# Kernel optimization log

Hardware: AMD Instinct MI355X
Metric: run time of the kernel (lower is better)

The kernel has to match this reference:

```python
import jax, jax.numpy as jnp
import numpy as np

P, L, D, H, K = 128, 800, 200, 100, 2  # passages, seq_len, input dim, hidden, spans per passage
VOCAB = 30522


def setup_inputs() -> dict:
    key = jax.random.key(0)
    ks = jax.random.split(key, 8)
    S_p = jax.random.normal(ks[0], (P, L, D), dtype=jnp.float32)
    # sorted along last axis so start <= end
    spans = jnp.sort(jax.random.randint(ks[1], (P, K, 2), 0, L), axis=-1)
    passages = jax.random.randint(ks[2], (P, L), 0, VOCAB)
    s = 0.05
    Wb = jax.random.normal(ks[3], (H, D), jnp.float32) * s
    We = jax.random.normal(ks[4], (H, D), jnp.float32) * s
    Wc = jax.random.normal(ks[5], (H, H), jnp.float32) * s
    Wo = jax.random.normal(ks[6], (H, H), jnp.float32) * s
    Wv = jax.random.normal(ks[7], (1, H), jnp.float32) * s
    return {"S_p": S_p, "spans": spans, "passages": passages,
            "Wb": Wb, "We": We, "Wc": Wc, "Wo": Wo, "Wv": Wv}


def reference(S_p, spans, passages, Wb, We, Wc, Wo, Wv):
    M = P * K
    p_idx = jnp.repeat(jnp.arange(P), K)            # [M] passage index per candidate
    starts = spans[:, :, 0].reshape(M)
    ends = spans[:, :, 1].reshape(M)
    t = jnp.arange(L)

    # S_Cs: candidate kept at its original position, zero elsewhere (== F.pad of the slice)
    span_mask = (t[None, :] >= starts[:, None]) & (t[None, :] <= ends[:, None])  # [M, L]
    S_Cs = S_p[p_idx] * span_mask[..., None].astype(S_p.dtype)                   # [M, L, D]

    # encoded candidates: token ids shifted to position 0, right-padded with 0
    gidx = jnp.clip(starts[:, None] + t[None, :], 0, L - 1)                      # [M, L]
    len_mask = t[None, :] <= (ends - starts)[:, None]
    encoded_candidates = jnp.where(len_mask, passages[p_idx[:, None], gidx], 0)  # [M, L]

    # condensed representation from start/end token states
    sb = S_p[p_idx, starts]                          # [M, D]
    se = S_p[p_idx, ends]                            # [M, D]
    r_Cs = jnp.tanh(sb @ Wb.T + se @ We.T)           # [M, H]

    # pairwise scores V_full[i, j] = Wv tanh(Wc r_i + Wo r_j)
    c = r_Cs @ Wc.T                                  # [M, H]
    o = r_Cs @ Wo.T                                  # [M, H]
    V_full = jnp.tanh(c[:, None, :] + o[None, :, :]) @ Wv[0]   # [M, M]

    # leave-one-out gather: V[i] = V_full[i, j != i]
    cols = jnp.arange(M - 1)
    rows = jnp.arange(M)
    idx = cols[None, :] + (cols[None, :] >= rows[:, None]).astype(cols.dtype)    # [M, M-1]
    V = V_full[rows[:, None], idx]                   # [M, M-1]

    # alpha[i] = exp(V[i]) / sum_{j != i} exp(V[j])  (per-column, non-standard normalization)
    E = jnp.exp(V)                                   # [M, M-1]
    denom = E.sum(axis=0, keepdims=True) - E
    alpha = E / denom                                # [M, M-1]

    # tilda_r[i] = sum over rows of (alpha excl row i) @ (r_Cs excl row i)
    s_rows = alpha.sum(axis=0, keepdims=True) - alpha   # [M, M-1]
    R_excl = r_Cs[idx]                                  # [M, M-1, H]
    tilda_r_Cs = jnp.einsum('mb,mbh->mh', s_rows, R_excl)  # [M, H]

    return S_Cs, r_Cs, encoded_candidates, V, tilda_r_Cs
```

## Files before the change

kernel.cpp:

```cpp
#include <hip/hip_runtime.h>
#include <math.h>

#define LP 800
#define DP 200
#define HP 100
#define MP 256
#define MM1 255

typedef float fx4 __attribute__((ext_vector_type(4)));

#define OFF_SCS  0u
#define OFF_R    40960000u
#define OFF_ENC  40985600u
#define OFF_V    41190400u
#define OFF_TIL  41255680u

#define WS_C     0u
#define WS_O     25600u
#define WS_S     51200u

__device__ __forceinline__ float tanh_fast(float x) {
    float e = __expf(2.0f * x);
    return 1.0f - 2.0f / (e + 1.0f);
}

__global__ __launch_bounds__(256) void scs_kernel(const fx4* __restrict__ Sp4,
                                                  const int* __restrict__ spans,
                                                  fx4* __restrict__ out4) {
    int m = blockIdx.y;
    int off = blockIdx.x * blockDim.x + threadIdx.x;
    if (off >= 40000) return;
    int p = m >> 1, k = m & 1;
    int start = spans[p * 4 + k * 2];
    int end   = spans[p * 4 + k * 2 + 1];
    int t = off / 50;
    fx4 v = (fx4)(0.f);
    if (t >= start && t <= end) v = Sp4[p * 40000 + off];
    __builtin_nontemporal_store(v, &out4[m * 40000 + off]);
}

__global__ __launch_bounds__(256) void encrco_kernel(const float* __restrict__ Sp,
                                                     const int* __restrict__ spans,
                                                     const int* __restrict__ passages,
                                                     const float* __restrict__ Wb,
                                                     const float* __restrict__ We,
                                                     const float* __restrict__ Wc,
                                                     const float* __restrict__ Wo,
                                                     float* __restrict__ enc,
                                                     float* __restrict__ r_out,
                                                     float* __restrict__ c_ws,
                                                     float* __restrict__ o_ws) {
    __shared__ float4 sb4[50], se4[50], rs4[25];
    int m = blockIdx.x;
    int p = m >> 1, k = m & 1;
    int start = spans[p * 4 + k * 2];
    int end   = spans[p * 4 + k * 2 + 1];
    int tid = threadIdx.x;

    int len = end - start;
    for (int t = tid; t < LP; t += 256) {
        int g = start + t; if (g > LP - 1) g = LP - 1;
        enc[m * LP + t] = (t <= len) ? (float)passages[p * LP + g] : 0.f;
    }

    const float4* sbp = (const float4*)(Sp + (size_t)(p * LP + start) * DP);
    const float4* sep = (const float4*)(Sp + (size_t)(p * LP + end) * DP);
    if (tid < 50)       sb4[tid]      = sbp[tid];
    else if (tid < 100) se4[tid - 50] = sep[tid - 50];
    __syncthreads();

    int h = tid;
    if (h < HP) {
        const float4* wb = (const float4*)(Wb + h * DP);
        const float4* we = (const float4*)(We + h * DP);
        float acc = 0.f;
        #pragma unroll
        for (int d = 0; d < 50; ++d) {
            float4 a = sb4[d], b = wb[d];
            acc += a.x * b.x + a.y * b.y + a.z * b.z + a.w * b.w;
            float4 a2 = se4[d], b2 = we[d];
            acc += a2.x * b2.x + a2.y * b2.y + a2.z * b2.z + a2.w * b2.w;
        }
        float r = tanh_fast(acc);
        ((float*)rs4)[h] = r;
        r_out[m * HP + h] = r;
    }
    __syncthreads();
    if (h < HP) {
        const float4* wc = (const float4*)(Wc + h * HP);
        const float4* wo = (const float4*)(Wo + h * HP);
        float accc = 0.f, acco = 0.f;
        #pragma unroll
        for (int q = 0; q < 25; ++q) {
            float4 r = rs4[q], cc = wc[q], oo = wo[q];
            accc += r.x * cc.x + r.y * cc.y + r.z * cc.z + r.w * cc.w;
            acco += r.x * oo.x + r.y * oo.y + r.z * oo.z + r.w * oo.w;
        }
        c_ws[m * HP + h] = accc;
        o_ws[m * HP + h] = acco;
    }
}

__global__ __launch_bounds__(256) void vcol_kernel(const float* __restrict__ c_ws,
                                                   const float* __restrict__ o_ws,
                                                   const float* __restrict__ Wv,
                                                   float* __restrict__ V_out,
                                                   float* __restrict__ s_ws) {
    __shared__ float4 olo4[25], ohi4[25], wv4[25];
    __shared__ float part[4];
    int jp = blockIdx.x;
    int i = threadIdx.x;
    if (i < 25) {
        olo4[i] = ((const float4*)(o_ws + jp * HP))[i];
        ohi4[i] = ((const float4*)(o_ws + (jp + 1) * HP))[i];
        wv4[i]  = ((const float4*)Wv)[i];
    }
    __syncthreads();

    const float4* c4p = (const float4*)(c_ws + i * HP);
    bool hi = (jp >= i);
    float acc = 0.f;
    #pragma unroll
    for (int q = 0; q < 25; ++q) {
        float4 c4 = c4p[q];
        float4 o4 = hi ? ohi4[q] : olo4[q];
        float4 w4 = wv4[q];
        acc += tanh_fast(c4.x + o4.x) * w4.x;
        acc += tanh_fast(c4.y + o4.y) * w4.y;
        acc += tanh_fast(c4.z + o4.z) * w4.z;
        acc += tanh_fast(c4.w + o4.w) * w4.w;
    }
    V_out[i * MM1 + jp] = acc;
    float e = __expf(acc);

    float v = e;
    v += __shfl_down(v, 32); v += __shfl_down(v, 16); v += __shfl_down(v, 8);
    v += __shfl_down(v, 4);  v += __shfl_down(v, 2);  v += __shfl_down(v, 1);
    if ((i & 63) == 0) part[i >> 6] = v;
    __syncthreads();
    float colE = part[0] + part[1] + part[2] + part[3];

    float a = e / (colE - e);

    __syncthreads();
    float v2 = a;
    v2 += __shfl_down(v2, 32); v2 += __shfl_down(v2, 16); v2 += __shfl_down(v2, 8);
    v2 += __shfl_down(v2, 4);  v2 += __shfl_down(v2, 2);  v2 += __shfl_down(v2, 1);
    if ((i & 63) == 0) part[i >> 6] = v2;
    __syncthreads();
    float colA = part[0] + part[1] + part[2] + part[3];

    s_ws[i * MM1 + jp] = colA - a;
}

__global__ __launch_bounds__(128) void tilda_kernel(const float* __restrict__ s_ws,
                                                    const float* __restrict__ r_out,
                                                    float* __restrict__ til_out) {
    __shared__ float s[MM1 + 1];
    int i = blockIdx.x;
    for (int jp = threadIdx.x; jp < MM1; jp += 128)
        s[jp] = s_ws[i * MM1 + jp];
    __syncthreads();
    int h = threadIdx.x;
    if (h < HP) {
        float acc = 0.f;
        #pragma unroll 4
        for (int jp = 0; jp < i; ++jp)
            acc += s[jp] * r_out[jp * HP + h];
        #pragma unroll 4
        for (int jp = i; jp < MM1; ++jp)
            acc += s[jp] * r_out[(jp + 1) * HP + h];
        til_out[i * HP + h] = acc;
    }
}

extern "C" void kernel_launch(void* const* d_in, const int* in_sizes, int n_in,
                              void* d_out, int out_size, void* d_ws, size_t ws_size,
                              hipStream_t stream) {
    const float* S_p      = (const float*)d_in[0];
    const int*   spans    = (const int*)d_in[1];
    const int*   passages = (const int*)d_in[2];
    const float* Wb       = (const float*)d_in[3];
    const float* We       = (const float*)d_in[4];
    const float* Wc       = (const float*)d_in[5];
    const float* Wo       = (const float*)d_in[6];
    const float* Wv       = (const float*)d_in[7];

    float* out = (float*)d_out;
    float* ws  = (float*)d_ws;

    float* out_scs = out + OFF_SCS;
    float* out_r   = out + OFF_R;
    float* out_enc = out + OFF_ENC;
    float* out_v   = out + OFF_V;
    float* out_til = out + OFF_TIL;

    float* ws_c = ws + WS_C;
    float* ws_o = ws + WS_O;
    float* ws_s = ws + WS_S;

    encrco_kernel<<<MP, 256, 0, stream>>>(S_p, spans, passages, Wb, We, Wc, Wo,
                                          out_enc, out_r, ws_c, ws_o);
    vcol_kernel<<<MM1, 256, 0, stream>>>(ws_c, ws_o, Wv, out_v, ws_s);
    tilda_kernel<<<MP, 128, 0, stream>>>(ws_s, out_r, out_til);

    dim3 gridA((40000 + 255) / 256, MP);
    scs_kernel<<<gridA, 256, 0, stream>>>((const fx4*)S_p, spans, (fx4*)out_scs);
}
```

Baseline: 276.9 us.

## Split S_Cs copy across the three dependent kernels to overlap small stages

Removes the standalone S_Cs masking kernel and spreads its 40000 blocks (one per 256 float4 writes) across the three dependent small kernels as extra blocks. The aim is to hide the latency-bound, low-occupancy encoder, pairwise-score and tilda stages behind the large bandwidth-bound copy. It also cuts one launch. The cost is per-element division to recover the candidate and offset from a flat index, and tilda blocks now run with 256 threads instead of 128.

```diff
diff --git a/kernel.cpp b/kernel.cpp
--- a/kernel.cpp
+++ b/kernel.cpp
@@ -19,37 +19,50 @@
 #define WS_O     25600u
 #define WS_S     51200u
 
+#define SCS_B1 13334
+#define SCS_B2 13333
+#define SCS_B3 13333
+#define NB1 0
+#define NB2 13334
+#define NB3 26667
+
 __device__ __forceinline__ float tanh_fast(float x) {
     float e = __expf(2.0f * x);
     return 1.0f - 2.0f / (e + 1.0f);
 }
 
-__global__ __launch_bounds__(256) void scs_kernel(const fx4* __restrict__ Sp4,
-                                                  const int* __restrict__ spans,
-                                                  fx4* __restrict__ out4) {
-    int m = blockIdx.y;
-    int off = blockIdx.x * blockDim.x + threadIdx.x;
-    if (off >= 40000) return;
-    int p = m >> 1, k = m & 1;
+__device__ __forceinline__ void scs_slice(const fx4* __restrict__ Sp4,
+                                          const int* __restrict__ spans,
+                                          fx4* __restrict__ out4,
+                                          unsigned ubase) {
+    unsigned u = ubase * 256u + threadIdx.x;
+    unsigned m = u / 40000u;
+    unsigned off = u - m * 40000u;
+    unsigned p = m >> 1, k = m & 1;
     int start = spans[p * 4 + k * 2];
     int end   = spans[p * 4 + k * 2 + 1];
-    int t = off / 50;
+    int t = (int)(off / 50u);
     fx4 v = (fx4)(0.f);
-    if (t >= start && t <= end) v = Sp4[p * 40000 + off];
-    __builtin_nontemporal_store(v, &out4[m * 40000 + off]);
-}
-
-__global__ __launch_bounds__(256) void encrco_kernel(const float* __restrict__ Sp,
-                                                     const int* __restrict__ spans,
-                                                     const int* __restrict__ passages,
-                                                     const float* __restrict__ Wb,
-                                                     const float* __restrict__ We,
-                                                     const float* __restrict__ Wc,
-                                                     const float* __restrict__ Wo,
-                                                     float* __restrict__ enc,
-                                                     float* __restrict__ r_out,
-                                                     float* __restrict__ c_ws,
-                                                     float* __restrict__ o_ws) {
+    if (t >= start && t <= end) v = Sp4[p * 40000u + off];
+    __builtin_nontemporal_store(v, &out4[m * 40000u + off]);
+}
+
+__global__ __launch_bounds__(256) void node1_kernel(const float* __restrict__ Sp,
+                                                    const int* __restrict__ spans,
+                                                    const int* __restrict__ passages,
+                                                    const float* __restrict__ Wb,
+                                                    const float* __restrict__ We,
+                                                    const float* __restrict__ Wc,
+                                                    const float* __restrict__ Wo,
+                                                    float* __restrict__ enc,
+                                                    float* __restrict__ r_out,
+                                                    float* __restrict__ c_ws,
+                                                    float* __restrict__ o_ws,
+                                                    fx4* __restrict__ out4) {
+    if (blockIdx.x >= MP) {
+        scs_slice((const fx4*)Sp, spans, out4, NB1 + blockIdx.x - MP);
+        return;
+    }
     __shared__ float4 sb4[50], se4[50], rs4[25];
     int m = blockIdx.x;
     int p = m >> 1, k = m & 1;
@@ -101,11 +114,18 @@
     }
 }
 
-__global__ __launch_bounds__(256) void vcol_kernel(const float* __restrict__ c_ws,
-                                                   const float* __restrict__ o_ws,
-                                                   const float* __restrict__ Wv,
-                                                   float* __restrict__ V_out,
-                                                   float* __restrict__ s_ws) {
+__global__ __launch_bounds__(256) void node2_kernel(const float* __restrict__ Sp,
+                                                    const int* __restrict__ spans,
+                                                    const float* __restrict__ c_ws,
+                                                    const float* __restrict__ o_ws,
+                                                    const float* __restrict__ Wv,
+                                                    float* __restrict__ V_out,
+                                                    float* __restrict__ s_ws,
+                                                    fx4* __restrict__ out4) {
+    if (blockIdx.x >= MM1) {
+        scs_slice((const fx4*)Sp, spans, out4, NB2 + blockIdx.x - MM1);
+        return;
+    }
     __shared__ float4 olo4[25], ohi4[25], wv4[25];
     __shared__ float part[4];
     int jp = blockIdx.x;
@@ -153,12 +173,19 @@
     s_ws[i * MM1 + jp] = colA - a;
 }
 
-__global__ __launch_bounds__(128) void tilda_kernel(const float* __restrict__ s_ws,
+__global__ __launch_bounds__(256) void node3_kernel(const float* __restrict__ Sp,
+                                                    const int* __restrict__ spans,
+                                                    const float* __restrict__ s_ws,
                                                     const float* __restrict__ r_out,
-                                                    float* __restrict__ til_out) {
+                                                    float* __restrict__ til_out,
+                                                    fx4* __restrict__ out4) {
+    if (blockIdx.x >= MP) {
+        scs_slice((const fx4*)Sp, spans, out4, NB3 + blockIdx.x - MP);
+        return;
+    }
     __shared__ float s[MM1 + 1];
     int i = blockIdx.x;
-    for (int jp = threadIdx.x; jp < MM1; jp += 128)
+    for (int jp = threadIdx.x; jp < MM1; jp += 256)
         s[jp] = s_ws[i * MM1 + jp];
     __syncthreads();
     int h = threadIdx.x;
@@ -199,11 +226,13 @@
     float* ws_o = ws + WS_O;
     float* ws_s = ws + WS_S;
 
-    encrco_kernel<<<MP, 256, 0, stream>>>(S_p, spans, passages, Wb, We, Wc, Wo,
-                                          out_enc, out_r, ws_c, ws_o);
-    vcol_kernel<<<MM1, 256, 0, stream>>>(ws_c, ws_o, Wv, out_v, ws_s);
-    tilda_kernel<<<MP, 128, 0, stream>>>(ws_s, out_r, out_til);
-
-    dim3 gridA((40000 + 255) / 256, MP);
-    scs_kernel<<<gridA, 256, 0, stream>>>((const fx4*)S_p, spans, (fx4*)out_scs);
-}
+    fx4* out4 = (fx4*)out_scs;
+
+    node1_kernel<<<MP + SCS_B1, 256, 0, stream>>>(S_p, spans, passages,
+                                                  Wb, We, Wc, Wo,
+                                                  out_enc, out_r, ws_c, ws_o, out4);
+    node2_kernel<<<MM1 + SCS_B2, 256, 0, stream>>>(S_p, spans, ws_c, ws_o, Wv,
+                                                   out_v, ws_s, out4);
+    node3_kernel<<<MP + SCS_B3, 256, 0, stream>>>(S_p, spans, ws_s, out_r,
+                                                  out_til, out4);
+}
```

Measured after the change: 267.1 us. -3.5%, faster.
